# Optimization experiments

Measured on AMD Instinct MI355X. Metric: run time of the kernel, lower is better.

## Reference

```python
import jax, jax.numpy as jnp
import numpy as np

D_MODEL = 1024
N_HEADS = 16
D_K = 64
BATCH = 2
SEQ = 2048
LN_EPS = 1e-5


def setup_inputs() -> dict:
    key = jax.random.key(0)
    ks = jax.random.split(key, 6)
    s = 1.0 / np.sqrt(D_MODEL)
    return {
        "h": jax.random.normal(ks[0], (BATCH, SEQ, D_MODEL), dtype=jnp.float32),
        "Wq": jax.random.normal(ks[1], (D_MODEL, D_MODEL), dtype=jnp.float32) * s,
        "bq": jnp.zeros((D_MODEL,), jnp.float32),
        "Wk": jax.random.normal(ks[2], (D_MODEL, D_MODEL), dtype=jnp.float32) * s,
        "bk": jnp.zeros((D_MODEL,), jnp.float32),
        "Wv": jax.random.normal(ks[3], (D_MODEL, D_MODEL), dtype=jnp.float32) * s,
        "bv": jnp.zeros((D_MODEL,), jnp.float32),
        "Wo": jax.random.normal(ks[4], (D_MODEL, D_MODEL), dtype=jnp.float32) * s,
        "bo": jnp.zeros((D_MODEL,), jnp.float32),
        "ln_w": jnp.ones((D_MODEL,), jnp.float32),
        "ln_b": jnp.zeros((D_MODEL,), jnp.float32),
    }


def _layernorm(x, w, b):
    mu = jnp.mean(x, axis=-1, keepdims=True)
    var = jnp.var(x, axis=-1, keepdims=True)
    return (x - mu) * jax.lax.rsqrt(var + LN_EPS) * w + b


def reference(h, Wq, bq, Wk, bk, Wv, bv, Wo, bo, ln_w, ln_b):
    b, s, _ = h.shape
    scale = 1.0 / np.sqrt(D_K)
    h_res = h
    hn = _layernorm(h, ln_w, ln_b)
    # Linear layers (torch convention: y = x @ W.T + b), split into heads
    q = (hn @ Wq.T + bq).reshape(b, s, N_HEADS, D_K)
    k = (hn @ Wk.T + bk).reshape(b, s, N_HEADS, D_K)
    v = (hn @ Wv.T + bv).reshape(b, s, N_HEADS, D_K)
    attn = jnp.einsum('bihd,bjhd->bhij', q, k) * scale  # [b, h, i, j]
    attn = jax.nn.softmax(attn, axis=-1)
    o = jnp.einsum('bhij,bjhd->bihd', attn, v).reshape(b, s, N_HEADS * D_K)
    out = o @ Wo.T + bo
    return out + h_res
```

## Files before the change

### kernel.cpp

```cpp
#include <hip/hip_runtime.h>
#include <cstdint>

#define D_MODEL 1024
#define N_HEADS 16
#define D_K     64
#define BATCH   2
#define SEQ     2048
#define TOKENS  (BATCH * SEQ)
#define LN_EPS  1e-5f
#define QSCALE  0.18033688011112042f

typedef __bf16 bf16x8 __attribute__((ext_vector_type(8)));
typedef float  floatx4  __attribute__((ext_vector_type(4)));
typedef float  floatx16 __attribute__((ext_vector_type(16)));
typedef float  floatx2  __attribute__((ext_vector_type(2)));
typedef unsigned uint32x2 __attribute__((ext_vector_type(2)));

__device__ __forceinline__ unsigned short f2bf(float f) {
  union { float f; unsigned u; } v; v.f = f;
  unsigned r = v.u + 0x7fffu + ((v.u >> 16) & 1u);
  return (unsigned short)(r >> 16);
}
__device__ __forceinline__ unsigned pk2bf(float hi, float lo) {
  union { float f; unsigned u; } a, b;
  a.f = hi; b.f = lo;
  return __builtin_amdgcn_perm(a.u, b.u, 0x07060302u);
}

__device__ __forceinline__ void cp16(void* lds, const void* g) {
  __builtin_amdgcn_global_load_lds(
      (__attribute__((address_space(1))) void*)g,
      (__attribute__((address_space(3))) void*)lds, 16, 0, 0);
}

__device__ __forceinline__ uint32x2 pswap(unsigned a, unsigned b) {
  return __builtin_amdgcn_permlane32_swap(a, b, false, false);
}

__global__ __launch_bounds__(256) void prep_kernel(
    const float* __restrict__ h, const float* __restrict__ w0,
    const float* __restrict__ w1, const float* __restrict__ w2,
    const float* __restrict__ w3, const float* __restrict__ lw,
    const float* __restrict__ lb, unsigned short* __restrict__ Wcat,
    unsigned short* __restrict__ hn) {
  if (blockIdx.x < 4096) {
    int wsel = blockIdx.x >> 10;
    const float* s = (wsel == 0) ? w0 : (wsel == 1) ? w1 : (wsel == 2) ? w2 : w3;
    unsigned short* d = Wcat + ((size_t)wsel << 20);
    int i = ((blockIdx.x & 1023) << 8) + threadIdx.x;
    float4 v = reinterpret_cast<const float4*>(s)[i];
    ushort4 o;
    o.x = f2bf(v.x); o.y = f2bf(v.y); o.z = f2bf(v.z); o.w = f2bf(v.w);
    reinterpret_cast<ushort4*>(d)[i] = o;
    return;
  }
  int row = blockIdx.x - 4096;
  const float* x = h + (size_t)row * D_MODEL;
  float4 v = reinterpret_cast<const float4*>(x)[threadIdx.x];
  float s  = v.x + v.y + v.z + v.w;
  float s2 = v.x * v.x + v.y * v.y + v.z * v.z + v.w * v.w;
  for (int m = 1; m < 64; m <<= 1) {
    s  += __shfl_xor(s, m);
    s2 += __shfl_xor(s2, m);
  }
  __shared__ float ls[4], ls2[4];
  int wave = threadIdx.x >> 6;
  if ((threadIdx.x & 63) == 0) { ls[wave] = s; ls2[wave] = s2; }
  __syncthreads();
  s  = ls[0] + ls[1] + ls[2] + ls[3];
  s2 = ls2[0] + ls2[1] + ls2[2] + ls2[3];
  float mu  = s * (1.0f / D_MODEL);
  float var = s2 * (1.0f / D_MODEL) - mu * mu;
  float rs  = rsqrtf(var + LN_EPS);
  float4 wv = reinterpret_cast<const float4*>(lw)[threadIdx.x];
  float4 bv = reinterpret_cast<const float4*>(lb)[threadIdx.x];
  ushort4 o;
  o.x = f2bf((v.x - mu) * rs * wv.x + bv.x);
  o.y = f2bf((v.y - mu) * rs * wv.y + bv.y);
  o.z = f2bf((v.z - mu) * rs * wv.z + bv.z);
  o.w = f2bf((v.w - mu) * rs * wv.w + bv.w);
  reinterpret_cast<ushort4*>(hn + (size_t)row * D_MODEL)[threadIdx.x] = o;
}

__global__ __launch_bounds__(512, 2) void gemm_qkv_kernel(
    const unsigned short* __restrict__ A, const unsigned short* __restrict__ Wcat,
    const float* __restrict__ bq, const float* __restrict__ bk,
    const float* __restrict__ bv,
    unsigned short* __restrict__ QK, unsigned short* __restrict__ VtG) {
  __shared__ unsigned short As[2][128 * 64];
  __shared__ unsigned short Bs[2][96 * 64];

  const int tid  = threadIdx.x;
  const int w    = tid >> 6;
  const int lane = tid & 63;
  const int l15  = lane & 15;
  const int quad = lane >> 4;
  const int sw   = l15 & 7;
  const int wrow = (w >> 1) * 32;
  const int wcol = (w & 1) * 48;

  const int flat  = blockIdx.x + (blockIdx.y << 5);
  const int swzid = ((flat & 7) << 7) + (flat >> 3);
  const int bm = (swzid >> 5) * 128;
  const int bn = (swzid & 31) * 96;

  const int srow = tid >> 3;
  const int swzc = (((tid & 7) ^ (srow & 7)) * 8);
  const unsigned short* ga = A    + (size_t)(bm + srow) * 1024 + swzc;
  const unsigned short* gb = Wcat + (size_t)(bn + srow) * 1024 + swzc;

  floatx4 acc[2][3];
#pragma unroll
  for (int i = 0; i < 2; ++i)
#pragma unroll
    for (int j = 0; j < 3; ++j) acc[i][j] = {0.f, 0.f, 0.f, 0.f};

  auto stage = [&](int k0, int b) {
    unsigned short* asl = &As[b][0] + w * 512;
#pragma unroll
    for (int i = 0; i < 2; ++i) cp16(asl + i * 4096, ga + (size_t)i * 64 * 1024 + k0);
    cp16(&Bs[b][0] + w * 512, gb + k0);
    if (w < 4) cp16(&Bs[b][0] + 4096 + w * 512, gb + (size_t)64 * 1024 + k0);
  };

  stage(0, 0);

  for (int t = 0; t < 16; ++t) {
    __syncthreads();
    if (t + 1 < 16) stage((t + 1) * 64, (t + 1) & 1);
    const unsigned short* Ab = &As[t & 1][0];
    const unsigned short* Bb = &Bs[t & 1][0];
#pragma unroll
    for (int kb = 0; kb < 2; ++kb) {
      bf16x8 af[2], bfr[3];
#pragma unroll
      for (int mi = 0; mi < 2; ++mi)
        af[mi] = *reinterpret_cast<const bf16x8*>(
            Ab + (wrow + mi * 16 + l15) * 64 + (((kb * 4 + quad) ^ sw) * 8));
#pragma unroll
      for (int ni = 0; ni < 3; ++ni)
        bfr[ni] = *reinterpret_cast<const bf16x8*>(
            Bb + (wcol + ni * 16 + l15) * 64 + (((kb * 4 + quad) ^ sw) * 8));
#pragma unroll
      for (int mi = 0; mi < 2; ++mi)
#pragma unroll
        for (int ni = 0; ni < 3; ++ni)
          acc[mi][ni] = __builtin_amdgcn_mfma_f32_16x16x32_bf16(af[mi], bfr[ni], acc[mi][ni], 0, 0, 0);
    }
  }

#pragma unroll
  for (int mi = 0; mi < 2; ++mi) {
    const int row0 = bm + wrow + mi * 16 + quad * 4;
#pragma unroll
    for (int ni = 0; ni < 3; ++ni) {
      const int cb  = bn + wcol + ni * 16;
      const int col = cb + l15;
      if (cb < 1024) {
        float bb = bq[col];
#pragma unroll
        for (int r = 0; r < 4; ++r)
          QK[(size_t)(row0 + r) * 2048 + col] = f2bf((acc[mi][ni][r] + bb) * QSCALE);
      } else if (cb < 2048) {
        float bb = bk[col - 1024];
#pragma unroll
        for (int r = 0; r < 4; ++r)
          QK[(size_t)(row0 + r) * 2048 + col] = f2bf(acc[mi][ni][r] + bb);
      } else {
        int d = col - 2048;
        float bb = bv[d];
        ushort4 o;
        o.x = f2bf(acc[mi][ni][0] + bb);
        o.y = f2bf(acc[mi][ni][1] + bb);
        o.z = f2bf(acc[mi][ni][2] + bb);
        o.w = f2bf(acc[mi][ni][3] + bb);
        *reinterpret_cast<ushort4*>(VtG + (size_t)d * 4096 + row0) = o;
      }
    }
  }
}

__global__ __launch_bounds__(256) void gemm_out_kernel(
    const unsigned short* __restrict__ A, const unsigned short* __restrict__ Bt,
    const float* __restrict__ bo, const float* __restrict__ resid,
    float* __restrict__ out) {
  __shared__ unsigned short As[2][128 * 64];
  __shared__ unsigned short Bs[2][64 * 64];

  const int tid  = threadIdx.x;
  const int w    = tid >> 6;
  const int lane = tid & 63;
  const int l15  = lane & 15;
  const int quad = lane >> 4;
  const int sw   = l15 & 7;
  const int wm = (w >> 1) * 64;
  const int wn = (w & 1) * 32;
  const int bm = blockIdx.y * 128;
  const int bn = blockIdx.x * 64;

  const int srow = tid >> 3;
  const int swzc = (((tid & 7) ^ (srow & 7)) * 8);
  const unsigned short* ga = A  + (size_t)(bm + srow) * 1024 + swzc;
  const unsigned short* gb = Bt + (size_t)(bn + srow) * 1024 + swzc;

  floatx4 acc[4][2];
  for (int i = 0; i < 4; ++i)
    for (int j = 0; j < 2; ++j) acc[i][j] = {0.f, 0.f, 0.f, 0.f};

  auto stage = [&](int k0, int b) {
    unsigned short* asl = &As[b][0] + w * 512;
    unsigned short* bsl = &Bs[b][0] + w * 512;
#pragma unroll
    for (int i = 0; i < 4; ++i) cp16(asl + i * 2048, ga + (size_t)i * 32 * 1024 + k0);
#pragma unroll
    for (int i = 0; i < 2; ++i) cp16(bsl + i * 2048, gb + (size_t)i * 32 * 1024 + k0);
  };

  stage(0, 0);

  for (int t = 0; t < 16; ++t) {
    __syncthreads();
    if (t + 1 < 16) stage((t + 1) * 64, (t + 1) & 1);
    const unsigned short* Ab = &As[t & 1][0];
    const unsigned short* Bb = &Bs[t & 1][0];
#pragma unroll
    for (int kb = 0; kb < 2; ++kb) {
      bf16x8 af[4], bfr[2];
#pragma unroll
      for (int mi = 0; mi < 4; ++mi)
        af[mi] = *reinterpret_cast<const bf16x8*>(
            Ab + (wm + mi * 16 + l15) * 64 + (((kb * 4 + quad) ^ sw) * 8));
#pragma unroll
      for (int ni = 0; ni < 2; ++ni)
        bfr[ni] = *reinterpret_cast<const bf16x8*>(
            Bb + (wn + ni * 16 + l15) * 64 + (((kb * 4 + quad) ^ sw) * 8));
#pragma unroll
      for (int mi = 0; mi < 4; ++mi)
#pragma unroll
        for (int ni = 0; ni < 2; ++ni)
          acc[mi][ni] = __builtin_amdgcn_mfma_f32_16x16x32_bf16(af[mi], bfr[ni], acc[mi][ni], 0, 0, 0);
    }
  }

#pragma unroll
  for (int mi = 0; mi < 4; ++mi)
#pragma unroll
    for (int ni = 0; ni < 2; ++ni) {
      int col = bn + wn + ni * 16 + l15;
      float bb = bo[col];
#pragma unroll
      for (int r = 0; r < 4; ++r) {
        int row = bm + wm + mi * 16 + quad * 4 + r;
        size_t idx = (size_t)row * 1024 + col;
        out[idx] = acc[mi][ni][r] + bb + resid[idx];
      }
    }
}

__global__ __launch_bounds__(512, 4) void attn_kernel(
    const unsigned short* __restrict__ QK, const unsigned short* __restrict__ VtG,
    unsigned short* __restrict__ O) {
  __shared__ unsigned short Ks[2][128 * 64];
  __shared__ unsigned short Vs[2][64 * 128];

  const int tid  = threadIdx.x;
  const int w    = tid >> 6;
  const int wq   = w & 3;
  const int kb0  = (w >> 2) * 2;
  const int lane = tid & 63;
  const int l31  = lane & 31;
  const int h    = lane >> 5;
  const int rsw  = (l31 & 7) ^ ((l31 >> 3) << 1);

  const int hh = blockIdx.x, qt = blockIdx.y, bz = blockIdx.z;
  const int tq0  = bz * SEQ + qt * 128;
  const int hoff = hh * 64;

  bf16x8 qf[4];
  {
    const unsigned short* qp =
        QK + (size_t)(tq0 + wq * 32 + l31) * 2048 + hoff + h * 8;
#pragma unroll
    for (int kd = 0; kd < 4; ++kd)
      qf[kd] = *reinterpret_cast<const bf16x8*>(qp + kd * 16);
  }

  floatx16 oacc[2];
#pragma unroll
  for (int db = 0; db < 2; ++db)
#pragma unroll
    for (int r = 0; r < 16; ++r) oacc[db][r] = 0.f;
  float lsum = 0.f;

  const unsigned short* kg = QK + 1024 + hoff
      + (size_t)(bz * SEQ + (tid >> 3)) * 2048
      + (((tid & 7) ^ ((tid >> 3) & 7) ^ ((w & 3) << 1)) * 8);
  const unsigned short* vg = VtG
      + (size_t)(hoff + (tid >> 4)) * 4096 + bz * SEQ
      + (((tid & 15) ^ ((tid >> 4) & 7) ^ (((w >> 1) & 3) << 1)) * 8);

  auto stage = [&](int kt, int b) {
    const unsigned short* kgi = kg + (size_t)(kt * 128) * 2048;
    const unsigned short* vgi = vg + kt * 128;
    unsigned short* ksl = Ks[b] + w * 512;
    unsigned short* vsl = Vs[b] + w * 512;
#pragma unroll
    for (int i = 0; i < 2; ++i) cp16(ksl + i * 4096, kgi + (size_t)(i * 64) * 2048);
#pragma unroll
    for (int i = 0; i < 2; ++i) cp16(vsl + i * 4096, vgi + (size_t)(i * 32) * 4096);
  };

  stage(0, 0);

  for (int kt = 0; kt < SEQ / 128; ++kt) {
    __syncthreads();
    if (kt + 1 < SEQ / 128) stage(kt + 1, (kt + 1) & 1);
    const unsigned short* Kb = Ks[kt & 1];
    const unsigned short* Vb = Vs[kt & 1];

    floatx16 ss[2];
#pragma unroll
    for (int kk = 0; kk < 2; ++kk)
#pragma unroll
      for (int r = 0; r < 16; ++r) ss[kk][r] = 0.f;
#pragma unroll
    for (int kk = 0; kk < 2; ++kk) {
      const int kb = kb0 + kk;
      const unsigned short* krow = Kb + (kb * 32 + l31) * 64;
#pragma unroll
      for (int kd = 0; kd < 4; ++kd) {
        bf16x8 kf = *reinterpret_cast<const bf16x8*>(
            krow + (((kd * 2 + h) ^ rsw) * 8));
        ss[kk] = __builtin_amdgcn_mfma_f32_32x32x16_bf16(kf, qf[kd], ss[kk], 0, 0, 0);
      }
    }

#pragma unroll
    for (int kk = 0; kk < 2; ++kk) {
      const int kb = kb0 + kk;
      float e[16];
#pragma unroll
      for (int r = 0; r < 16; ++r) e[r] = __builtin_amdgcn_exp2f(ss[kk][r]);
      floatx2 a0 = {e[0], e[1]},   a1 = {e[2], e[3]},
              a2 = {e[4], e[5]},   a3 = {e[6], e[7]},
              a4 = {e[8], e[9]},   a5 = {e[10], e[11]},
              a6 = {e[12], e[13]}, a7 = {e[14], e[15]};
      floatx2 b0 = a0 + a1, b1 = a2 + a3, b2 = a4 + a5, b3 = a6 + a7;
      floatx2 c0 = b0 + b1, c1 = b2 + b3;
      floatx2 d2 = c0 + c1;
      float bs = d2.x + d2.y;
      {
        union { float f; unsigned u; } bu; bu.f = bs;
        uint32x2 br = pswap(bu.u, bu.u);
        union { unsigned u; float f; } b0u, b1u;
        b0u.u = br.x; b1u.u = br.y;
        bs = b0u.f + b1u.f;
      }
      lsum += bs;
      unsigned p[8];
#pragma unroll
      for (int i = 0; i < 8; ++i) p[i] = pk2bf(e[2 * i + 1], e[2 * i]);

#pragma unroll
      for (int sub = 0; sub < 2; ++sub) {
        uint32x2 r0 = pswap(p[sub * 4 + 0], p[sub * 4 + 2]);
        uint32x2 r1 = pswap(p[sub * 4 + 1], p[sub * 4 + 3]);
        union { unsigned u[4]; bf16x8 v; } pf;
        pf.u[0] = r0.x;
        pf.u[1] = r1.x;
        pf.u[2] = r0.y;
        pf.u[3] = r1.y;
#pragma unroll
        for (int db = 0; db < 2; ++db) {
          bf16x8 vf = *reinterpret_cast<const bf16x8*>(
              Vb + (db * 32 + l31) * 128 + (((kb * 4 + sub * 2 + h) ^ rsw) * 8));
          oacc[db] = __builtin_amdgcn_mfma_f32_32x32x16_bf16(vf, pf.v, oacc[db], 0, 0, 0);
        }
      }
    }
  }

  __syncthreads();
  float* osc = (float*)&Ks[0][0];
  float* lsc = (float*)&Vs[0][0];
  if (w >= 4) {
    float* dst = osc + ((size_t)(wq * 64 + lane) * 32);
#pragma unroll
    for (int db = 0; db < 2; ++db)
#pragma unroll
      for (int r = 0; r < 16; ++r)
        dst[(db * 16 + r + lane) & 31] = oacc[db][r];
    lsc[wq * 64 + lane] = lsum;
  }
  __syncthreads();
  if (w < 4) {
    const float* src = osc + ((size_t)(wq * 64 + lane) * 32);
    lsum += lsc[wq * 64 + lane];
#pragma unroll
    for (int db = 0; db < 2; ++db)
#pragma unroll
      for (int r = 0; r < 16; ++r)
        oacc[db][r] += src[(db * 16 + r + lane) & 31];

    float inv = 1.0f / lsum;
    unsigned short* ob = O + (size_t)(tq0 + wq * 32 + l31) * 1024 + hoff;
#pragma unroll
    for (int db = 0; db < 2; ++db)
#pragma unroll
      for (int rg = 0; rg < 4; ++rg) {
        int d0 = db * 32 + rg * 8 + h * 4;
        uint2 ov;
        ov.x = pk2bf(oacc[db][rg * 4 + 1] * inv, oacc[db][rg * 4 + 0] * inv);
        ov.y = pk2bf(oacc[db][rg * 4 + 3] * inv, oacc[db][rg * 4 + 2] * inv);
        *reinterpret_cast<uint2*>(ob + d0) = ov;
      }
  }
}

extern "C" void kernel_launch(void* const* d_in, const int* in_sizes, int n_in,
                              void* d_out, int out_size, void* d_ws, size_t ws_size,
                              hipStream_t stream) {
  const float* h    = (const float*)d_in[0];
  const float* Wq   = (const float*)d_in[1];
  const float* bq   = (const float*)d_in[2];
  const float* Wk   = (const float*)d_in[3];
  const float* bk   = (const float*)d_in[4];
  const float* Wv   = (const float*)d_in[5];
  const float* bv   = (const float*)d_in[6];
  const float* Wo   = (const float*)d_in[7];
  const float* bo   = (const float*)d_in[8];
  const float* ln_w = (const float*)d_in[9];
  const float* ln_b = (const float*)d_in[10];
  float* out = (float*)d_out;

  unsigned short* ws = (unsigned short*)d_ws;
  const size_t WSZ = (size_t)1 << 20;
  unsigned short* Wcat = ws;
  unsigned short* hn   = Wcat + 4 * WSZ;
  unsigned short* QKb  = hn + (size_t)TOKENS * D_MODEL;
  unsigned short* VtG  = QKb + (size_t)TOKENS * 2048;
  unsigned short* Obuf = VtG + (size_t)D_MODEL * TOKENS;

  prep_kernel<<<8192, 256, 0, stream>>>(h, Wq, Wk, Wv, Wo, ln_w, ln_b, Wcat, hn);

  gemm_qkv_kernel<<<dim3(32, 32), 512, 0, stream>>>(hn, Wcat, bq, bk, bv, QKb, VtG);

  attn_kernel<<<dim3(N_HEADS, SEQ / 128, BATCH), 512, 0, stream>>>(QKb, VtG, Obuf);

  gemm_out_kernel<<<dim3(16, 32), 256, 0, stream>>>(Obuf, Wcat + 3 * WSZ, bo, h, out);
}
```

Measured before the change: 196.1 us.

## Halve attention query tile and load K fragments directly from global memory

The attention block now covers 64 queries instead of 128, doubling the grid, and splits the 128-key tile four ways across warps instead of two. K is no longer staged in shared memory; each warp reads its K fragments straight from global into registers, and only V stays double-buffered in LDS. The cross-warp reduction now merges four partial outputs in two passes through the freed LDS. The aim is more blocks, lower LDS use and higher occupancy, at the cost of twice the K/V global traffic per query and unhidden global-load latency for K.

```diff
diff --git a/kernel.cpp b/kernel.cpp
--- a/kernel.cpp
+++ b/kernel.cpp
@@ -260,20 +260,19 @@
 __global__ __launch_bounds__(512, 4) void attn_kernel(
     const unsigned short* __restrict__ QK, const unsigned short* __restrict__ VtG,
     unsigned short* __restrict__ O) {
-  __shared__ unsigned short Ks[2][128 * 64];
   __shared__ unsigned short Vs[2][64 * 128];
 
   const int tid  = threadIdx.x;
   const int w    = tid >> 6;
-  const int wq   = w & 3;
-  const int kb0  = (w >> 2) * 2;
+  const int wq   = w & 1;
+  const int kq   = w >> 1;
   const int lane = tid & 63;
   const int l31  = lane & 31;
   const int h    = lane >> 5;
   const int rsw  = (l31 & 7) ^ ((l31 >> 3) << 1);
 
   const int hh = blockIdx.x, qt = blockIdx.y, bz = blockIdx.z;
-  const int tq0  = bz * SEQ + qt * 128;
+  const int tq0  = bz * SEQ + qt * 64;
   const int hoff = hh * 64;
 
   bf16x8 qf[4];
@@ -285,6 +284,9 @@
       qf[kd] = *reinterpret_cast<const bf16x8*>(qp + kd * 16);
   }
 
+  const unsigned short* kgr = QK + 1024 + hoff
+      + (size_t)(bz * SEQ + kq * 32 + l31) * 2048 + h * 8;
+
   floatx16 oacc[2];
 #pragma unroll
   for (int db = 0; db < 2; ++db)
@@ -292,116 +294,115 @@
     for (int r = 0; r < 16; ++r) oacc[db][r] = 0.f;
   float lsum = 0.f;
 
-  const unsigned short* kg = QK + 1024 + hoff
-      + (size_t)(bz * SEQ + (tid >> 3)) * 2048
-      + (((tid & 7) ^ ((tid >> 3) & 7) ^ ((w & 3) << 1)) * 8);
   const unsigned short* vg = VtG
       + (size_t)(hoff + (tid >> 4)) * 4096 + bz * SEQ
       + (((tid & 15) ^ ((tid >> 4) & 7) ^ (((w >> 1) & 3) << 1)) * 8);
 
-  auto stage = [&](int kt, int b) {
-    const unsigned short* kgi = kg + (size_t)(kt * 128) * 2048;
+  auto stageV = [&](int kt, int b) {
     const unsigned short* vgi = vg + kt * 128;
-    unsigned short* ksl = Ks[b] + w * 512;
     unsigned short* vsl = Vs[b] + w * 512;
-#pragma unroll
-    for (int i = 0; i < 2; ++i) cp16(ksl + i * 4096, kgi + (size_t)(i * 64) * 2048);
 #pragma unroll
     for (int i = 0; i < 2; ++i) cp16(vsl + i * 4096, vgi + (size_t)(i * 32) * 4096);
   };
 
-  stage(0, 0);
+  stageV(0, 0);
 
   for (int kt = 0; kt < SEQ / 128; ++kt) {
     __syncthreads();
-    if (kt + 1 < SEQ / 128) stage(kt + 1, (kt + 1) & 1);
-    const unsigned short* Kb = Ks[kt & 1];
+    bf16x8 kf[4];
+    {
+      const unsigned short* kgi = kgr + (size_t)(kt * 128) * 2048;
+#pragma unroll
+      for (int kd = 0; kd < 4; ++kd)
+        kf[kd] = *reinterpret_cast<const bf16x8*>(kgi + kd * 16);
+    }
+    if (kt + 1 < SEQ / 128) stageV(kt + 1, (kt + 1) & 1);
     const unsigned short* Vb = Vs[kt & 1];
 
-    floatx16 ss[2];
-#pragma unroll
-    for (int kk = 0; kk < 2; ++kk)
-#pragma unroll
-      for (int r = 0; r < 16; ++r) ss[kk][r] = 0.f;
-#pragma unroll
-    for (int kk = 0; kk < 2; ++kk) {
-      const int kb = kb0 + kk;
-      const unsigned short* krow = Kb + (kb * 32 + l31) * 64;
-#pragma unroll
-      for (int kd = 0; kd < 4; ++kd) {
-        bf16x8 kf = *reinterpret_cast<const bf16x8*>(
-            krow + (((kd * 2 + h) ^ rsw) * 8));
-        ss[kk] = __builtin_amdgcn_mfma_f32_32x32x16_bf16(kf, qf[kd], ss[kk], 0, 0, 0);
+    floatx16 ss;
+#pragma unroll
+    for (int r = 0; r < 16; ++r) ss[r] = 0.f;
+#pragma unroll
+    for (int kd = 0; kd < 4; ++kd)
+      ss = __builtin_amdgcn_mfma_f32_32x32x16_bf16(kf[kd], qf[kd], ss, 0, 0, 0);
+
+    float e[16];
+#pragma unroll
+    for (int r = 0; r < 16; ++r) e[r] = __builtin_amdgcn_exp2f(ss[r]);
+    floatx2 a0 = {e[0], e[1]},   a1 = {e[2], e[3]},
+            a2 = {e[4], e[5]},   a3 = {e[6], e[7]},
+            a4 = {e[8], e[9]},   a5 = {e[10], e[11]},
+            a6 = {e[12], e[13]}, a7 = {e[14], e[15]};
+    floatx2 b0 = a0 + a1, b1 = a2 + a3, b2 = a4 + a5, b3 = a6 + a7;
+    floatx2 c0 = b0 + b1, c1 = b2 + b3;
+    floatx2 d2 = c0 + c1;
+    float bs = d2.x + d2.y;
+    {
+      union { float f; unsigned u; } bu; bu.f = bs;
+      uint32x2 br = pswap(bu.u, bu.u);
+      union { unsigned u; float f; } b0u, b1u;
+      b0u.u = br.x; b1u.u = br.y;
+      bs = b0u.f + b1u.f;
+    }
+    lsum += bs;
+    unsigned p[8];
+#pragma unroll
+    for (int i = 0; i < 8; ++i) p[i] = pk2bf(e[2 * i + 1], e[2 * i]);
+
+#pragma unroll
+    for (int sub = 0; sub < 2; ++sub) {
+      uint32x2 r0 = pswap(p[sub * 4 + 0], p[sub * 4 + 2]);
+      uint32x2 r1 = pswap(p[sub * 4 + 1], p[sub * 4 + 3]);
+      union { unsigned u[4]; bf16x8 v; } pf;
+      pf.u[0] = r0.x;
+      pf.u[1] = r1.x;
+      pf.u[2] = r0.y;
+      pf.u[3] = r1.y;
+#pragma unroll
+      for (int db = 0; db < 2; ++db) {
+        bf16x8 vf = *reinterpret_cast<const bf16x8*>(
+            Vb + (db * 32 + l31) * 128 + (((kq * 4 + sub * 2 + h) ^ rsw) * 8));
+        oacc[db] = __builtin_amdgcn_mfma_f32_32x32x16_bf16(vf, pf.v, oacc[db], 0, 0, 0);
       }
     }
-
-#pragma unroll
-    for (int kk = 0; kk < 2; ++kk) {
-      const int kb = kb0 + kk;
-      float e[16];
-#pragma unroll
-      for (int r = 0; r < 16; ++r) e[r] = __builtin_amdgcn_exp2f(ss[kk][r]);
-      floatx2 a0 = {e[0], e[1]},   a1 = {e[2], e[3]},
-              a2 = {e[4], e[5]},   a3 = {e[6], e[7]},
-              a4 = {e[8], e[9]},   a5 = {e[10], e[11]},
-              a6 = {e[12], e[13]}, a7 = {e[14], e[15]};
-      floatx2 b0 = a0 + a1, b1 = a2 + a3, b2 = a4 + a5, b3 = a6 + a7;
-      floatx2 c0 = b0 + b1, c1 = b2 + b3;
-      floatx2 d2 = c0 + c1;
-      float bs = d2.x + d2.y;
-      {
-        union { float f; unsigned u; } bu; bu.f = bs;
-        uint32x2 br = pswap(bu.u, bu.u);
-        union { unsigned u; float f; } b0u, b1u;
-        b0u.u = br.x; b1u.u = br.y;
-        bs = b0u.f + b1u.f;
-      }
-      lsum += bs;
-      unsigned p[8];
-#pragma unroll
-      for (int i = 0; i < 8; ++i) p[i] = pk2bf(e[2 * i + 1], e[2 * i]);
-
-#pragma unroll
-      for (int sub = 0; sub < 2; ++sub) {
-        uint32x2 r0 = pswap(p[sub * 4 + 0], p[sub * 4 + 2]);
-        uint32x2 r1 = pswap(p[sub * 4 + 1], p[sub * 4 + 3]);
-        union { unsigned u[4]; bf16x8 v; } pf;
-        pf.u[0] = r0.x;
-        pf.u[1] = r1.x;
-        pf.u[2] = r0.y;
-        pf.u[3] = r1.y;
-#pragma unroll
-        for (int db = 0; db < 2; ++db) {
-          bf16x8 vf = *reinterpret_cast<const bf16x8*>(
-              Vb + (db * 32 + l31) * 128 + (((kb * 4 + sub * 2 + h) ^ rsw) * 8));
-          oacc[db] = __builtin_amdgcn_mfma_f32_32x32x16_bf16(vf, pf.v, oacc[db], 0, 0, 0);
-        }
-      }
-    }
-  }
+  }
+
+  float* osc = (float*)&Vs[0][0];
+  float* lsc = osc + 6144;
+  const int slot  = (kq - 1) * 128 + wq * 64 + lane;
+  const int rslot = wq * 64 + lane;
 
   __syncthreads();
-  float* osc = (float*)&Ks[0][0];
-  float* lsc = (float*)&Vs[0][0];
-  if (w >= 4) {
-    float* dst = osc + ((size_t)(wq * 64 + lane) * 32);
-#pragma unroll
-    for (int db = 0; db < 2; ++db)
-#pragma unroll
-      for (int r = 0; r < 16; ++r)
-        dst[(db * 16 + r + lane) & 31] = oacc[db][r];
-    lsc[wq * 64 + lane] = lsum;
+  if (kq > 0) {
+    float* dst = osc + (size_t)slot * 16;
+#pragma unroll
+    for (int r = 0; r < 16; ++r) dst[(r + lane) & 15] = oacc[0][r];
+    lsc[slot] = lsum;
   }
   __syncthreads();
-  if (w < 4) {
-    const float* src = osc + ((size_t)(wq * 64 + lane) * 32);
-    lsum += lsc[wq * 64 + lane];
-#pragma unroll
-    for (int db = 0; db < 2; ++db)
-#pragma unroll
-      for (int r = 0; r < 16; ++r)
-        oacc[db][r] += src[(db * 16 + r + lane) & 31];
-
+  if (kq == 0) {
+    lsum += lsc[rslot] + lsc[128 + rslot] + lsc[256 + rslot];
+#pragma unroll
+    for (int gi = 0; gi < 3; ++gi) {
+      const float* src = osc + (size_t)(gi * 128 + rslot) * 16;
+#pragma unroll
+      for (int r = 0; r < 16; ++r) oacc[0][r] += src[(r + lane) & 15];
+    }
+  }
+  __syncthreads();
+  if (kq > 0) {
+    float* dst = osc + (size_t)slot * 16;
+#pragma unroll
+    for (int r = 0; r < 16; ++r) dst[(r + lane) & 15] = oacc[1][r];
+  }
+  __syncthreads();
+  if (kq == 0) {
+#pragma unroll
+    for (int gi = 0; gi < 3; ++gi) {
+      const float* src = osc + (size_t)(gi * 128 + rslot) * 16;
+#pragma unroll
+      for (int r = 0; r < 16; ++r) oacc[1][r] += src[(r + lane) & 15];
+    }
     float inv = 1.0f / lsum;
     unsigned short* ob = O + (size_t)(tq0 + wq * 32 + l31) * 1024 + hoff;
 #pragma unroll
@@ -445,7 +446,7 @@
 
   gemm_qkv_kernel<<<dim3(32, 32), 512, 0, stream>>>(hn, Wcat, bq, bk, bv, QKb, VtG);
 
-  attn_kernel<<<dim3(N_HEADS, SEQ / 128, BATCH), 512, 0, stream>>>(QKb, VtG, Obuf);
+  attn_kernel<<<dim3(N_HEADS, SEQ / 64, BATCH), 512, 0, stream>>>(QKb, VtG, Obuf);
 
   gemm_out_kernel<<<dim3(16, 32), 256, 0, stream>>>(Obuf, Wcat + 3 * WSZ, bo, h, out);
 }
```

After: 231.8 us. +18.2%, slower.
